# Performance work log

Hardware: AMD Instinct MI355X
Metric: run time of the kernel (lower is better)

## Reference

```python
import jax, jax.numpy as jnp
import numpy as np

N = 2048      # total nodes across all graphs
G = 16        # number of graphs
IN = 16       # input_dim
D = 256       # hidden_dim (d_model)
NH = 8        # num_heads
HD = D // NH  # head_dim
FF = 4 * D    # dim_feedforward
L = 4         # num_layers
LAT = 32      # latent_dim
BH = D // 2   # beta_head hidden
LN_EPS = 1e-5


def setup_inputs() -> dict:
    key = jax.random.key(0)
    ks = jax.random.split(key, 32)

    def w(k, shape, fan_in):
        return jax.random.normal(k, shape, jnp.float32) * (1.0 / np.sqrt(fan_in))

    inp = {
        "x": jax.random.normal(ks[0], (N, IN), jnp.float32),
        "coords": jax.random.normal(ks[1], (N, 3), jnp.float32),
        "batch": jnp.sort(jax.random.randint(ks[2], (N,), 0, G)).astype(jnp.int32),
        # input projection
        "Wi": w(ks[3], (IN, D), IN), "bi": jnp.zeros((D,), jnp.float32),
        # per-layer transformer params, stacked on leading layer dim
        "qkv_w": w(ks[4], (L, D, 3 * D), D), "qkv_b": jnp.zeros((L, 3 * D), jnp.float32),
        "out_w": w(ks[5], (L, D, D), D),     "out_b": jnp.zeros((L, D), jnp.float32),
        "ff1_w": w(ks[6], (L, D, FF), D),    "ff1_b": jnp.zeros((L, FF), jnp.float32),
        "ff2_w": w(ks[7], (L, FF, D), FF),   "ff2_b": jnp.zeros((L, D), jnp.float32),
        "ln1_s": jnp.ones((L, D), jnp.float32), "ln1_b": jnp.zeros((L, D), jnp.float32),
        "ln2_s": jnp.ones((L, D), jnp.float32), "ln2_b": jnp.zeros((L, D), jnp.float32),
        # heads
        "lat_w": w(ks[8], (D, LAT), D), "lat_b": jnp.zeros((LAT,), jnp.float32),
        "b1_w": w(ks[9], (D, BH), D),   "b1_b": jnp.zeros((BH,), jnp.float32),
        "b2_w": w(ks[10], (BH, 1), BH), "b2_b": jnp.zeros((1,), jnp.float32),
    }
    return inp


def _layer_norm(h, s, b):
    m = jnp.mean(h, axis=-1, keepdims=True)
    v = jnp.mean(jnp.square(h - m), axis=-1, keepdims=True)
    return (h - m) * jax.lax.rsqrt(v + LN_EPS) * s + b


def _forward(x, batch, Wi, bi, qkv_w, qkv_b, out_w, out_b, ff1_w, ff1_b,
             ff2_w, ff2_b, ln1_s, ln1_b, ln2_s, ln2_b, lat_w, lat_b,
             b1_w, b1_b, b2_w, b2_b):
    n = x.shape[0]
    h = x @ Wi + bi  # [N, D]
    # the per-graph python loop in torch == block-diagonal attention mask
    attn_bias = jnp.where(batch[:, None] == batch[None, :], 0.0, -1e9).astype(h.dtype)  # [N, N]
    scale = 1.0 / np.sqrt(HD)
    for l in range(L):
        qkv = h @ qkv_w[l] + qkv_b[l]                 # [N, 3D]
        q, k, v = jnp.split(qkv, 3, axis=-1)
        q = q.reshape(n, NH, HD)
        k = k.reshape(n, NH, HD)
        v = v.reshape(n, NH, HD)
        scores = jnp.einsum('nhd,mhd->hnm', q, k) * scale + attn_bias[None]  # [H, N, N]
        a = jax.nn.softmax(scores, axis=-1)
        o = jnp.einsum('hnm,mhd->nhd', a, v).reshape(n, D)
        o = o @ out_w[l] + out_b[l]
        h = _layer_norm(h + o, ln1_s[l], ln1_b[l])     # post-norm (torch default)
        f = jax.nn.relu(h @ ff1_w[l] + ff1_b[l]) @ ff2_w[l] + ff2_b[l]
        h = _layer_norm(h + f, ln2_s[l], ln2_b[l])
    lat = h @ lat_w + lat_b                            # [N, LAT]
    norm = jnp.maximum(jnp.linalg.norm(lat, axis=-1, keepdims=True), 1e-12)
    lat = lat / norm * np.sqrt(LAT)
    beta = jax.nn.sigmoid(jax.nn.relu(h @ b1_w + b1_b) @ b2_w + b2_b)  # [N, 1]
    beta = jnp.clip(beta, 1e-6, 1.0 - 1e-6)
    return beta, lat


def reference(x, coords, batch, Wi, bi, qkv_w, qkv_b, out_w, out_b,
              ff1_w, ff1_b, ff2_w, ff2_b, ln1_s, ln1_b, ln2_s, ln2_b,
              lat_w, lat_b, b1_w, b1_b, b2_w, b2_b):
    # coords is accepted (signature fidelity) but unused in the original forward
    del coords
    return _forward(x, batch, Wi, bi, qkv_w, qkv_b, out_w, out_b, ff1_w, ff1_b,
                    ff2_w, ff2_b, ln1_s, ln1_b, ln2_s, ln2_b, lat_w, lat_b,
                    b1_w, b1_b, b2_w, b2_b)
```

## Files before the change

### kernel.cpp

```cpp
#include <hip/hip_runtime.h>
#include <hip/hip_bf16.h>

typedef __attribute__((ext_vector_type(8))) short bf16x8;
typedef __attribute__((ext_vector_type(4))) float f32x4;

__device__ inline float wave_sum64(float v) {
#pragma unroll
  for (int m = 32; m >= 1; m >>= 1) v += __shfl_xor(v, m, 64);
  return v;
}
__device__ inline ushort f2bf(float f) {
  uint u = __float_as_uint(f);
  return (ushort)((u + 0x7FFFu + ((u >> 16) & 1u)) >> 16);
}

__global__ __launch_bounds__(256) void pack_inproj(
    const float* __restrict__ qkv_w, const float* __restrict__ out_w,
    const float* __restrict__ ff1_w, const float* __restrict__ ff2_w,
    const float* __restrict__ b1_w, const float* __restrict__ lat_w,
    short* __restrict__ qkv_t, short* __restrict__ out_t,
    short* __restrict__ ff1_t, short* __restrict__ ff2_t,
    short* __restrict__ b1_t, short* __restrict__ lat_t,
    const int* __restrict__ batch, int* __restrict__ starts, int* __restrict__ meta,
    const float* __restrict__ x, const float* __restrict__ Wi,
    const float* __restrict__ bi, float* __restrict__ h, short* __restrict__ hb) {
  int t = blockIdx.x;
  __shared__ float tile[32][33];

  if (t >= 3113) {
    const int row = t - 3113;
    const int j = threadIdx.x;
    float* xs = &tile[0][0];
    if (j < 16) xs[j] = x[(size_t)row * 16 + j];
    __syncthreads();
    float acc = bi[j];
#pragma unroll
    for (int k = 0; k < 16; ++k) acc += xs[k] * Wi[k * 256 + j];
    h[(size_t)row * 256 + j] = acc;
    hb[(size_t)row * 256 + j] = (short)f2bf(acc);
    return;
  }
  if (t == 3112) {
    for (int i = threadIdx.x; i < 2048; i += 256) {
      int b = batch[i];
      if (i == 0) {
        for (int g = 0; g <= b; ++g) starts[g] = 0;
      } else {
        int bp = batch[i - 1];
        for (int g = bp + 1; g <= b; ++g) starts[g] = i;
      }
      if (i == 2047) {
        for (int g = b + 1; g <= 16; ++g) starts[g] = 2048;
      }
    }
    __syncthreads();
    if (threadIdx.x == 0) {
      int nt = 0;
      for (int g = 0; g < 16; ++g) {
        const int js = starts[g], je = starts[g + 1];
        for (int q0 = js; q0 < je; q0 += 16) {
          meta[1 + nt * 3] = q0;
          meta[2 + nt * 3] = js;
          meta[3 + nt * 3] = je;
          ++nt;
        }
      }
      meta[0] = nt;
    }
    return;
  }
  const float* src;
  short* dst;
  int Kd, Nd, rem;
  if (t < 768) {
    int l = t / 192; rem = t % 192; Kd = 256; Nd = 768;
    src = qkv_w + (size_t)l * Kd * Nd; dst = qkv_t + (size_t)l * Nd * Kd;
  } else if (t < 1024) {
    t -= 768; int l = t / 64; rem = t % 64; Kd = 256; Nd = 256;
    src = out_w + (size_t)l * Kd * Nd; dst = out_t + (size_t)l * Nd * Kd;
  } else if (t < 2048) {
    t -= 1024; int l = t / 256; rem = t % 256; Kd = 256; Nd = 1024;
    src = ff1_w + (size_t)l * Kd * Nd; dst = ff1_t + (size_t)l * Nd * Kd;
  } else if (t < 3072) {
    t -= 2048; int l = t / 256; rem = t % 256; Kd = 1024; Nd = 256;
    src = ff2_w + (size_t)l * Kd * Nd; dst = ff2_t + (size_t)l * Nd * Kd;
  } else if (t < 3104) {
    rem = t - 3072; Kd = 256; Nd = 128; src = b1_w; dst = b1_t;
  } else {
    rem = t - 3104; Kd = 256; Nd = 32; src = lat_w; dst = lat_t;
  }
  const int ntn = Nd / 32;
  const int kt = rem / ntn, nt = rem % ntn;
  const int tx = threadIdx.x & 31, ty = threadIdx.x >> 5;
#pragma unroll
  for (int r = 0; r < 4; ++r) {
    int k = kt * 32 + ty + r * 8;
    tile[ty + r * 8][tx] = src[(size_t)k * Nd + nt * 32 + tx];
  }
  __syncthreads();
#pragma unroll
  for (int r = 0; r < 4; ++r) {
    int n = nt * 32 + ty + r * 8;
    dst[(size_t)n * Kd + kt * 32 + tx] = (short)f2bf(tile[tx][ty + r * 8]);
  }
}

template <int ACT, int P, int VT>
__global__ __launch_bounds__(256) void gemm_bf16(
    const short* __restrict__ A, const short* __restrict__ Bt,
    const float* __restrict__ bias, float* __restrict__ Cf, short* __restrict__ Cb,
    short* __restrict__ vtg, int M, int N, int K, int kpb) {
  __shared__ short As[64 * 128];
  __shared__ short Bs[64 * 128];

  const int t = threadIdx.x;
  const int bm = blockIdx.y, bn = blockIdx.x, bz = blockIdx.z;
  const int srow = t >> 2, sq = t & 3;
  const int lane = t & 63, wid = t >> 6;
  const int wr = wid >> 1, wc = wid & 1;
  const int fr = lane & 15, fs = lane >> 4;
  const int rx = srow & 7;

  f32x4 acc[2][2];
#pragma unroll
  for (int m = 0; m < 2; ++m)
#pragma unroll
    for (int n = 0; n < 2; ++n) acc[m][n] = (f32x4){0.f, 0.f, 0.f, 0.f};

  const int kbase = bz * kpb;
  const short* ap = A + (size_t)(bm * 64 + srow) * K + kbase;
  const int ng = bn * 64 + srow;
  const short* bp = Bt + (size_t)ng * K + kbase;
  const int ar0 = wr * 32 + fr, ar1 = ar0 + 16;
  const int bc0 = wc * 32 + fr, bc1 = bc0 + 16;

  for (int k0 = 0; k0 < kpb; k0 += 128) {
    bf16x8 av[4], bv[4];
#pragma unroll
    for (int i = 0; i < 4; ++i) av[i] = *(const bf16x8*)(ap + k0 + (sq * 4 + i) * 8);
    if (ng < N) {
#pragma unroll
      for (int i = 0; i < 4; ++i) bv[i] = *(const bf16x8*)(bp + k0 + (sq * 4 + i) * 8);
    } else {
#pragma unroll
      for (int i = 0; i < 4; ++i) bv[i] = (bf16x8){0, 0, 0, 0, 0, 0, 0, 0};
    }
    __syncthreads();
#pragma unroll
    for (int i = 0; i < 4; ++i) {
      const int s = sq * 4 + i;
      *(bf16x8*)(As + srow * 128 + ((s ^ rx) * 8)) = av[i];
      *(bf16x8*)(Bs + srow * 128 + ((s ^ rx) * 8)) = bv[i];
    }
    __syncthreads();
#pragma unroll
    for (int ks = 0; ks < 4; ++ks) {
      const int u = ks * 4 + fs;
      bf16x8 a0 = *(const bf16x8*)(As + ar0 * 128 + ((u ^ (ar0 & 7)) * 8));
      bf16x8 a1 = *(const bf16x8*)(As + ar1 * 128 + ((u ^ (ar1 & 7)) * 8));
      bf16x8 b0 = *(const bf16x8*)(Bs + bc0 * 128 + ((u ^ (bc0 & 7)) * 8));
      bf16x8 b1 = *(const bf16x8*)(Bs + bc1 * 128 + ((u ^ (bc1 & 7)) * 8));
      acc[0][0] = __builtin_amdgcn_mfma_f32_16x16x32_bf16(a0, b0, acc[0][0], 0, 0, 0);
      acc[0][1] = __builtin_amdgcn_mfma_f32_16x16x32_bf16(a0, b1, acc[0][1], 0, 0, 0);
      acc[1][0] = __builtin_amdgcn_mfma_f32_16x16x32_bf16(a1, b0, acc[1][0], 0, 0, 0);
      acc[1][1] = __builtin_amdgcn_mfma_f32_16x16x32_bf16(a1, b1, acc[1][1], 0, 0, 0);
    }
  }

  if (P == 0) {
    if (!(VT && bn >= 8)) {
#pragma unroll
      for (int n = 0; n < 2; ++n) {
        const int col = bn * 64 + wc * 32 + n * 16 + fr;
        if (col < N) {
          const float bvv = bias[col];
#pragma unroll
          for (int m = 0; m < 2; ++m) {
            const int rbase = bm * 64 + wr * 32 + m * 16 + fs * 4;
#pragma unroll
            for (int j = 0; j < 4; ++j) {
              float v = acc[m][n][j] + bvv;
              if (ACT == 1) v = fmaxf(v, 0.f);
              Cb[(size_t)(rbase + j) * N + col] = (short)f2bf(v);
            }
          }
        }
      }
    }
    if (VT && bn >= 8) {
      short* tr = As;
      __syncthreads();
#pragma unroll
      for (int n = 0; n < 2; ++n) {
        const int c = wc * 32 + n * 16 + fr;
        const float bvv = bias[bn * 64 + c];
#pragma unroll
        for (int m = 0; m < 2; ++m)
#pragma unroll
          for (int j = 0; j < 4; ++j) {
            const int r = wr * 32 + m * 16 + fs * 4 + j;
            tr[c * 68 + r] = (short)f2bf(acc[m][n][j] + bvv);
          }
      }
      __syncthreads();
      const int tx = t & 63, ty = t >> 6;
      const int d0 = bn * 64 - 512, rb = bm * 64;
#pragma unroll
      for (int r = 0; r < 16; ++r) {
        const int d = ty * 16 + r;
        vtg[(size_t)(d0 + d) * 2048 + rb + tx] = tr[d * 68 + tx];
      }
    }
  } else {
#pragma unroll
    for (int n = 0; n < 2; ++n) {
      const int col = bn * 64 + wc * 32 + n * 16 + fr;
      const float bvv = (bz == 0) ? bias[col] : 0.f;
#pragma unroll
      for (int m = 0; m < 2; ++m) {
        const int rbase = bm * 64 + wr * 32 + m * 16 + fs * 4;
#pragma unroll
        for (int j = 0; j < 4; ++j) {
          Cf[(size_t)(bz * M + rbase + j) * N + col] = acc[m][n][j] + bvv;
        }
      }
    }
  }
}

__global__ __launch_bounds__(512) void attn_fused(
    const short* __restrict__ qkv, const short* __restrict__ vtg,
    const int* __restrict__ meta, const short* __restrict__ out_t,
    const float* __restrict__ outb, const float* __restrict__ lns,
    const float* __restrict__ lnb, float* __restrict__ h, short* __restrict__ hb) {
  __shared__ short Ot[8][16][40];
  __shared__ float redS[8][16], redQ[8][16];
  const int w = threadIdx.x >> 6;
  const int tile = blockIdx.x;
  const bool active = (tile < meta[0]);
  const int lane = threadIdx.x & 63;
  const int fr = lane & 15, fs = lane >> 4;
  const int q0 = active ? meta[1 + tile * 3] : 0;
  const int js = active ? meta[2 + tile * 3] : 0;
  const int je = active ? meta[3 + tile * 3] : 0;
  const int jbase = js & ~15;
  const int njt = active ? ((je - jbase + 15) >> 4) : 0;
  const float scale = 0.17677669529663687f;

  const int qrow = min(q0 + fr, 2047);
  const bf16x8 qf = *(const bf16x8*)(qkv + (size_t)qrow * 768 + w * 32 + fs * 8);
  const int jeq = (q0 + fr < je) ? je : 0;

  f32x4 s[16];
#pragma unroll
  for (int jt = 0; jt < 16; ++jt)
    s[jt] = (f32x4){-3.0e38f, -3.0e38f, -3.0e38f, -3.0e38f};

#pragma unroll
  for (int jt = 0; jt < 16; ++jt) {
    if (jt < njt) {
      const int krow = min(jbase + jt * 16 + fr, 2047);
      const bf16x8 kf = *(const bf16x8*)(qkv + (size_t)krow * 768 + 256 + w * 32 + fs * 8);
      s[jt] = __builtin_amdgcn_mfma_f32_16x16x32_bf16(
          kf, qf, (f32x4){0.f, 0.f, 0.f, 0.f}, 0, 0, 0);
    }
  }
  float mx = -3.0e38f;
#pragma unroll
  for (int jt = 0; jt < 16; ++jt) {
    if (jt < njt) {
#pragma unroll
      for (int jj = 0; jj < 4; ++jj) {
        const int j = jbase + jt * 16 + fs * 4 + jj;
        const bool valid = (j >= js) && (j < jeq);
        s[jt][jj] = valid ? s[jt][jj] * scale : -3.0e38f;
        mx = fmaxf(mx, s[jt][jj]);
      }
    }
  }
  mx = fmaxf(mx, __shfl_xor(mx, 16, 64));
  mx = fmaxf(mx, __shfl_xor(mx, 32, 64));
  float l = 0.f;
#pragma unroll
  for (int jt = 0; jt < 16; ++jt) {
#pragma unroll
    for (int jj = 0; jj < 4; ++jj) {
      const float p = __expf(s[jt][jj] - mx);
      s[jt][jj] = p;
      l += p;
    }
  }
  l += __shfl_xor(l, 16, 64);
  l += __shfl_xor(l, 32, 64);

  f32x4 oa[2];
  oa[0] = (f32x4){0.f, 0.f, 0.f, 0.f};
  oa[1] = (f32x4){0.f, 0.f, 0.f, 0.f};
#pragma unroll
  for (int p2 = 0; p2 < 8; ++p2) {
    if (p2 * 2 < njt) {
      bf16x8 pa;
      pa[0] = (short)f2bf(s[p2 * 2][0]);     pa[1] = (short)f2bf(s[p2 * 2][1]);
      pa[2] = (short)f2bf(s[p2 * 2][2]);     pa[3] = (short)f2bf(s[p2 * 2][3]);
      pa[4] = (short)f2bf(s[p2 * 2 + 1][0]); pa[5] = (short)f2bf(s[p2 * 2 + 1][1]);
      pa[6] = (short)f2bf(s[p2 * 2 + 1][2]); pa[7] = (short)f2bf(s[p2 * 2 + 1][3]);
      const int jb0 = min(jbase + p2 * 32 + fs * 4, 2044);
      const int jb1 = min(jbase + p2 * 32 + 16 + fs * 4, 2044);
#pragma unroll
      for (int nt = 0; nt < 2; ++nt) {
        const short* vrow = vtg + (size_t)(w * 32 + nt * 16 + fr) * 2048;
        const short4 v0 = *(const short4*)(vrow + jb0);
        const short4 v1 = *(const short4*)(vrow + jb1);
        bf16x8 vf;
        vf[0] = v0.x; vf[1] = v0.y; vf[2] = v0.z; vf[3] = v0.w;
        vf[4] = v1.x; vf[5] = v1.y; vf[6] = v1.z; vf[7] = v1.w;
        oa[nt] = __builtin_amdgcn_mfma_f32_16x16x32_bf16(pa, vf, oa[nt], 0, 0, 0);
      }
    }
  }

#pragma unroll
  for (int jj = 0; jj < 4; ++jj) {
    const float lq = __shfl(l, fs * 4 + jj, 64);
    const float inv = (lq > 0.f) ? (1.f / lq) : 0.f;
    const int q = fs * 4 + jj;
    Ot[w][q][fr] = (short)f2bf(oa[0][jj] * inv);
    Ot[w][q][16 + fr] = (short)f2bf(oa[1][jj] * inv);
  }
  __syncthreads();

  f32x4 acc2[2];
  acc2[0] = (f32x4){0.f, 0.f, 0.f, 0.f};
  acc2[1] = (f32x4){0.f, 0.f, 0.f, 0.f};
#pragma unroll
  for (int ks = 0; ks < 8; ++ks) {
    const bf16x8 afrag = *(const bf16x8*)&Ot[ks][fr][fs * 8];
#pragma unroll
    for (int nt2 = 0; nt2 < 2; ++nt2) {
      const int col_row = (w * 2 + nt2) * 16 + fr;
      const bf16x8 bfrag =
          *(const bf16x8*)(out_t + (size_t)col_row * 256 + ks * 32 + fs * 8);
      acc2[nt2] = __builtin_amdgcn_mfma_f32_16x16x32_bf16(afrag, bfrag, acc2[nt2], 0, 0, 0);
    }
  }

  float d[2][4], ps[4], pq[4];
#pragma unroll
  for (int jj = 0; jj < 4; ++jj) {
    const int node = q0 + fs * 4 + jj;
    const int noder = min(node, 2047);
#pragma unroll
    for (int nt2 = 0; nt2 < 2; ++nt2) {
      const int col = w * 32 + nt2 * 16 + fr;
      d[nt2][jj] = acc2[nt2][jj] + outb[col] + h[(size_t)noder * 256 + col];
    }
    ps[jj] = d[0][jj] + d[1][jj];
    pq[jj] = d[0][jj] * d[0][jj] + d[1][jj] * d[1][jj];
#pragma unroll
    for (int m = 1; m <= 8; m <<= 1) {
      ps[jj] += __shfl_xor(ps[jj], m, 64);
      pq[jj] += __shfl_xor(pq[jj], m, 64);
    }
  }
  if (fr == 0) {
#pragma unroll
    for (int jj = 0; jj < 4; ++jj) {
      redS[w][fs * 4 + jj] = ps[jj];
      redQ[w][fs * 4 + jj] = pq[jj];
    }
  }
  __syncthreads();

#pragma unroll
  for (int jj = 0; jj < 4; ++jj) {
    const int row = fs * 4 + jj;
    float S = 0.f, Q = 0.f;
#pragma unroll
    for (int ww = 0; ww < 8; ++ww) { S += redS[ww][row]; Q += redQ[ww][row]; }
    const float mean = S * (1.f / 256.f);
    const float var = Q * (1.f / 256.f) - mean * mean;
    const float rs = rsqrtf(var + 1e-5f);
    const int node = q0 + row;
    if (active && node < je) {
#pragma unroll
      for (int nt2 = 0; nt2 < 2; ++nt2) {
        const int col = w * 32 + nt2 * 16 + fr;
        const float o = (d[nt2][jj] - mean) * rs * lns[col] + lnb[col];
        h[(size_t)node * 256 + col] = o;
        hb[(size_t)node * 256 + col] = (short)f2bf(o);
      }
    }
  }
}

template <int P>
__global__ __launch_bounds__(256) void ln_kernel(
    const float* __restrict__ base, const float* __restrict__ delta,
    const float* __restrict__ s, const float* __restrict__ b,
    float* __restrict__ outf, short* __restrict__ outb) {
  const int row = blockIdx.x * 4 + (threadIdx.x >> 6);
  const int lane = threadIdx.x & 63;
  float4 v = *(const float4*)(base + (size_t)row * 256 + lane * 4);
#pragma unroll
  for (int p = 0; p < P; ++p) {
    const float4 xb = *(const float4*)(delta + (size_t)(p * 2048 + row) * 256 + lane * 4);
    v.x += xb.x; v.y += xb.y; v.z += xb.z; v.w += xb.w;
  }
  float sum = wave_sum64(v.x + v.y + v.z + v.w);
  const float mean = sum * (1.f / 256.f);
  float4 d = make_float4(v.x - mean, v.y - mean, v.z - mean, v.w - mean);
  float sq = wave_sum64(d.x * d.x + d.y * d.y + d.z * d.z + d.w * d.w);
  const float rs = rsqrtf(sq * (1.f / 256.f) + 1e-5f);
  const float4 sv = *(const float4*)(s + lane * 4);
  const float4 bv = *(const float4*)(b + lane * 4);
  float4 o = make_float4(d.x * rs * sv.x + bv.x, d.y * rs * sv.y + bv.y,
                         d.z * rs * sv.z + bv.z, d.w * rs * sv.w + bv.w);
  *(float4*)(outf + (size_t)row * 256 + lane * 4) = o;
  short4 ob;
  ob.x = (short)f2bf(o.x); ob.y = (short)f2bf(o.y);
  ob.z = (short)f2bf(o.z); ob.w = (short)f2bf(o.w);
  *(short4*)(outb + (size_t)row * 256 + lane * 4) = ob;
}

__global__ __launch_bounds__(256) void heads_kernel(
    const short* __restrict__ A, const short* __restrict__ lat_t,
    const float* __restrict__ lat_b, float* __restrict__ lat_out,
    const short* __restrict__ b1_t, const float* __restrict__ b1b,
    const float* __restrict__ w2, const float* __restrict__ b2b,
    float* __restrict__ beta) {
  __shared__ short smem[64 * 128 * 2];
  const int t = threadIdx.x;
  const int lane = t & 63, w = t >> 6;
  const int fr = lane & 15, fs = lane >> 4;

  if (blockIdx.x < 32) {
    short* As = smem;
    short* Bs = smem + 64 * 128;
    const int bm = blockIdx.x;
    const int srow = t >> 2, sq = t & 3;
    const int rx = srow & 7;
    f32x4 acc[2];
    acc[0] = (f32x4){0.f, 0.f, 0.f, 0.f};
    acc[1] = (f32x4){0.f, 0.f, 0.f, 0.f};
    const short* ap = A + (size_t)(bm * 64 + srow) * 256;
    const short* bp = lat_t + (size_t)srow * 256;
    const int ar = w * 16 + fr;
    for (int k0 = 0; k0 < 256; k0 += 128) {
      bf16x8 av[4], bv[4];
#pragma unroll
      for (int i = 0; i < 4; ++i) av[i] = *(const bf16x8*)(ap + k0 + (sq * 4 + i) * 8);
      if (srow < 32) {
#pragma unroll
        for (int i = 0; i < 4; ++i) bv[i] = *(const bf16x8*)(bp + k0 + (sq * 4 + i) * 8);
      } else {
#pragma unroll
        for (int i = 0; i < 4; ++i) bv[i] = (bf16x8){0, 0, 0, 0, 0, 0, 0, 0};
      }
      __syncthreads();
#pragma unroll
      for (int i = 0; i < 4; ++i) {
        const int s = sq * 4 + i;
        *(bf16x8*)(As + srow * 128 + ((s ^ rx) * 8)) = av[i];
        *(bf16x8*)(Bs + srow * 128 + ((s ^ rx) * 8)) = bv[i];
      }
      __syncthreads();
#pragma unroll
      for (int ks = 0; ks < 4; ++ks) {
        const int u = ks * 4 + fs;
        bf16x8 a0 = *(const bf16x8*)(As + ar * 128 + ((u ^ (ar & 7)) * 8));
        bf16x8 b0 = *(const bf16x8*)(Bs + fr * 128 + ((u ^ (fr & 7)) * 8));
        bf16x8 b1 = *(const bf16x8*)(Bs + (16 + fr) * 128 + ((u ^ ((16 + fr) & 7)) * 8));
        acc[0] = __builtin_amdgcn_mfma_f32_16x16x32_bf16(a0, b0, acc[0], 0, 0, 0);
        acc[1] = __builtin_amdgcn_mfma_f32_16x16x32_bf16(a0, b1, acc[1], 0, 0, 0);
      }
    }
    const float b0v = lat_b[fr], b1v = lat_b[16 + fr];
#pragma unroll
    for (int j = 0; j < 4; ++j) {
      const int row = bm * 64 + w * 16 + fs * 4 + j;
      float v0 = acc[0][j] + b0v;
      float v1 = acc[1][j] + b1v;
      float ss = v0 * v0 + v1 * v1;
      ss += __shfl_xor(ss, 1, 64);
      ss += __shfl_xor(ss, 2, 64);
      ss += __shfl_xor(ss, 4, 64);
      ss += __shfl_xor(ss, 8, 64);
      const float inv = 5.656854249492381f / fmaxf(sqrtf(ss), 1e-12f);
      lat_out[(size_t)row * 32 + fr] = v0 * inv;
      lat_out[(size_t)row * 32 + 16 + fr] = v1 * inv;
    }
  } else {
    float* red = (float*)smem;
    const int rb = (blockIdx.x - 32) * 16;
    f32x4 acc[2];
    acc[0] = (f32x4){0.f, 0.f, 0.f, 0.f};
    acc[1] = (f32x4){0.f, 0.f, 0.f, 0.f};
    const short* ap = A + (size_t)(rb + fr) * 256;
    const short* bp = b1_t + (size_t)(w * 32 + fr) * 256;
    for (int k0 = 0; k0 < 256; k0 += 32) {
      const bf16x8 af = *(const bf16x8*)(ap + k0 + fs * 8);
#pragma unroll
      for (int n = 0; n < 2; ++n) {
        const bf16x8 bf = *(const bf16x8*)(bp + (size_t)n * 16 * 256 + k0 + fs * 8);
        acc[n] = __builtin_amdgcn_mfma_f32_16x16x32_bf16(af, bf, acc[n], 0, 0, 0);
      }
    }
    const int c0 = w * 32 + fr, c1 = c0 + 16;
    const float b0 = b1b[c0], b1 = b1b[c1];
    const float w0 = w2[c0], w1 = w2[c1];
    float part[4];
#pragma unroll
    for (int j = 0; j < 4; ++j) {
      const float d0 = fmaxf(acc[0][j] + b0, 0.f);
      const float d1 = fmaxf(acc[1][j] + b1, 0.f);
      part[j] = d0 * w0 + d1 * w1;
#pragma unroll
      for (int m = 1; m <= 8; m <<= 1) part[j] += __shfl_xor(part[j], m, 64);
    }
    if (fr == 0) {
#pragma unroll
      for (int j = 0; j < 4; ++j) red[w * 16 + fs * 4 + j] = part[j];
    }
    __syncthreads();
    if (t < 16) {
      const float S = red[t] + red[16 + t] + red[32 + t] + red[48 + t] + b2b[0];
      float sgm = 1.f / (1.f + __expf(-S));
      sgm = fminf(fmaxf(sgm, 1e-6f), 1.f - 1e-6f);
      beta[rb + t] = sgm;
    }
  }
}

extern "C" void kernel_launch(void* const* d_in, const int* in_sizes, int n_in,
                              void* d_out, int out_size, void* d_ws, size_t ws_size,
                              hipStream_t stream) {
  const int N = 2048, D = 256, FF = 1024, L = 4;

  const float* x     = (const float*)d_in[0];
  const int*   batch = (const int*)d_in[2];
  const float* Wi    = (const float*)d_in[3];
  const float* bi    = (const float*)d_in[4];
  const float* qkv_w = (const float*)d_in[5];
  const float* qkv_b = (const float*)d_in[6];
  const float* out_w = (const float*)d_in[7];
  const float* out_b = (const float*)d_in[8];
  const float* ff1_w = (const float*)d_in[9];
  const float* ff1_b = (const float*)d_in[10];
  const float* ff2_w = (const float*)d_in[11];
  const float* ff2_b = (const float*)d_in[12];
  const float* ln1_s = (const float*)d_in[13];
  const float* ln1_b = (const float*)d_in[14];
  const float* ln2_s = (const float*)d_in[15];
  const float* ln2_b = (const float*)d_in[16];
  const float* lat_w = (const float*)d_in[17];
  const float* lat_b = (const float*)d_in[18];
  const float* b1_w  = (const float*)d_in[19];
  const float* b1_b  = (const float*)d_in[20];
  const float* b2_w  = (const float*)d_in[21];
  const float* b2_b  = (const float*)d_in[22];

  float* ws = (float*)d_ws;
  float* h      = ws;
  float* tmp    = h + (size_t)N * D;
  int*  starts  = (int*)(tmp + (size_t)4 * N * D);
  int*  meta    = starts + 32;
  short* hb     = (short*)(meta + 448);
  short* qkvb   = hb + (size_t)N * D;
  short* ffb    = qkvb + (size_t)N * 3 * D;
  short* vtg    = ffb + (size_t)N * FF;
  short* qkv_t  = vtg + (size_t)256 * 2048;
  short* out_t  = qkv_t + (size_t)L * 768 * 256;
  short* ff1_t  = out_t + (size_t)L * 256 * 256;
  short* ff2_t  = ff1_t + (size_t)L * 1024 * 256;
  short* b1_t   = ff2_t + (size_t)L * 256 * 1024;
  short* lat_t  = b1_t + (size_t)128 * 256;

  float* beta_out = (float*)d_out;
  float* lat_out  = beta_out + N;

  pack_inproj<<<3113 + 2048, 256, 0, stream>>>(
      qkv_w, out_w, ff1_w, ff2_w, b1_w, lat_w,
      qkv_t, out_t, ff1_t, ff2_t, b1_t, lat_t,
      batch, starts, meta, x, Wi, bi, h, hb);

  for (int l = 0; l < L; ++l) {
    gemm_bf16<0, 0, 1><<<dim3(12, 32, 1), 256, 0, stream>>>(
        hb, qkv_t + (size_t)l * 768 * 256, qkv_b + (size_t)l * 768,
        nullptr, qkvb, vtg, N, 768, 256, 256);
    attn_fused<<<144, 512, 0, stream>>>(
        qkvb, vtg, meta, out_t + (size_t)l * 256 * 256, out_b + (size_t)l * 256,
        ln1_s + (size_t)l * D, ln1_b + (size_t)l * D, h, hb);
    gemm_bf16<1, 0, 0><<<dim3(16, 32, 1), 256, 0, stream>>>(
        hb, ff1_t + (size_t)l * FF * 256, ff1_b + (size_t)l * FF,
        nullptr, ffb, nullptr, N, FF, 256, 256);
    gemm_bf16<0, 4, 0><<<dim3(4, 32, 4), 256, 0, stream>>>(
        ffb, ff2_t + (size_t)l * 256 * FF, ff2_b + (size_t)l * 256,
        tmp, nullptr, nullptr, N, 256, 1024, 256);
    ln_kernel<4><<<N / 4, 256, 0, stream>>>(
        h, tmp, ln2_s + (size_t)l * D, ln2_b + (size_t)l * D, h, hb);
  }

  heads_kernel<<<160, 256, 0, stream>>>(hb, lat_t, lat_b, lat_out,
                                        b1_t, b1_b, b2_w, b2_b, beta_out);
}
```

Measured before the change: 190.5 us.

## Fuse FF1, ReLU, FF2, residual and LayerNorm into one per-row-tile kernel

Replaces the FF1 GEMM, the split-K FF2 GEMM and the LayerNorm kernel with a single kernel per 16-row tile. The ReLU intermediate is held in shared memory and the residual-plus-LayerNorm epilogue is done in registers. This removes two launches per layer and the global round trips of the 1024-wide intermediate and the split-K partials. In exchange, only 128 blocks run, weights are read straight from global memory without LDS tiling, and every block re-reads the full FF weights. The generic GEMM is also specialised into a QKV-only kernel.

```diff
diff --git a/kernel.cpp b/kernel.cpp
--- a/kernel.cpp
+++ b/kernel.cpp
@@ -105,16 +105,15 @@
   }
 }
 
-template <int ACT, int P, int VT>
-__global__ __launch_bounds__(256) void gemm_bf16(
+__global__ __launch_bounds__(256) void gemm_qkv(
     const short* __restrict__ A, const short* __restrict__ Bt,
-    const float* __restrict__ bias, float* __restrict__ Cf, short* __restrict__ Cb,
-    short* __restrict__ vtg, int M, int N, int K, int kpb) {
+    const float* __restrict__ bias, short* __restrict__ Cb,
+    short* __restrict__ vtg, int N, int K) {
   __shared__ short As[64 * 128];
   __shared__ short Bs[64 * 128];
 
   const int t = threadIdx.x;
-  const int bm = blockIdx.y, bn = blockIdx.x, bz = blockIdx.z;
+  const int bm = blockIdx.y, bn = blockIdx.x;
   const int srow = t >> 2, sq = t & 3;
   const int lane = t & 63, wid = t >> 6;
   const int wr = wid >> 1, wc = wid & 1;
@@ -127,24 +126,18 @@
 #pragma unroll
     for (int n = 0; n < 2; ++n) acc[m][n] = (f32x4){0.f, 0.f, 0.f, 0.f};
 
-  const int kbase = bz * kpb;
-  const short* ap = A + (size_t)(bm * 64 + srow) * K + kbase;
+  const short* ap = A + (size_t)(bm * 64 + srow) * K;
   const int ng = bn * 64 + srow;
-  const short* bp = Bt + (size_t)ng * K + kbase;
+  const short* bp = Bt + (size_t)ng * K;
   const int ar0 = wr * 32 + fr, ar1 = ar0 + 16;
   const int bc0 = wc * 32 + fr, bc1 = bc0 + 16;
 
-  for (int k0 = 0; k0 < kpb; k0 += 128) {
+  for (int k0 = 0; k0 < K; k0 += 128) {
     bf16x8 av[4], bv[4];
 #pragma unroll
     for (int i = 0; i < 4; ++i) av[i] = *(const bf16x8*)(ap + k0 + (sq * 4 + i) * 8);
-    if (ng < N) {
-#pragma unroll
-      for (int i = 0; i < 4; ++i) bv[i] = *(const bf16x8*)(bp + k0 + (sq * 4 + i) * 8);
-    } else {
-#pragma unroll
-      for (int i = 0; i < 4; ++i) bv[i] = (bf16x8){0, 0, 0, 0, 0, 0, 0, 0};
-    }
+#pragma unroll
+    for (int i = 0; i < 4; ++i) bv[i] = *(const bf16x8*)(bp + k0 + (sq * 4 + i) * 8);
     __syncthreads();
 #pragma unroll
     for (int i = 0; i < 4; ++i) {
@@ -167,63 +160,42 @@
     }
   }
 
-  if (P == 0) {
-    if (!(VT && bn >= 8)) {
-#pragma unroll
-      for (int n = 0; n < 2; ++n) {
-        const int col = bn * 64 + wc * 32 + n * 16 + fr;
-        if (col < N) {
-          const float bvv = bias[col];
-#pragma unroll
-          for (int m = 0; m < 2; ++m) {
-            const int rbase = bm * 64 + wr * 32 + m * 16 + fs * 4;
-#pragma unroll
-            for (int j = 0; j < 4; ++j) {
-              float v = acc[m][n][j] + bvv;
-              if (ACT == 1) v = fmaxf(v, 0.f);
-              Cb[(size_t)(rbase + j) * N + col] = (short)f2bf(v);
-            }
-          }
-        }
-      }
-    }
-    if (VT && bn >= 8) {
-      short* tr = As;
-      __syncthreads();
-#pragma unroll
-      for (int n = 0; n < 2; ++n) {
-        const int c = wc * 32 + n * 16 + fr;
-        const float bvv = bias[bn * 64 + c];
-#pragma unroll
-        for (int m = 0; m < 2; ++m)
-#pragma unroll
-          for (int j = 0; j < 4; ++j) {
-            const int r = wr * 32 + m * 16 + fs * 4 + j;
-            tr[c * 68 + r] = (short)f2bf(acc[m][n][j] + bvv);
-          }
-      }
-      __syncthreads();
-      const int tx = t & 63, ty = t >> 6;
-      const int d0 = bn * 64 - 512, rb = bm * 64;
-#pragma unroll
-      for (int r = 0; r < 16; ++r) {
-        const int d = ty * 16 + r;
-        vtg[(size_t)(d0 + d) * 2048 + rb + tx] = tr[d * 68 + tx];
-      }
-    }
-  } else {
+  if (bn < 8) {
 #pragma unroll
     for (int n = 0; n < 2; ++n) {
       const int col = bn * 64 + wc * 32 + n * 16 + fr;
-      const float bvv = (bz == 0) ? bias[col] : 0.f;
+      const float bvv = bias[col];
 #pragma unroll
       for (int m = 0; m < 2; ++m) {
         const int rbase = bm * 64 + wr * 32 + m * 16 + fs * 4;
 #pragma unroll
         for (int j = 0; j < 4; ++j) {
-          Cf[(size_t)(bz * M + rbase + j) * N + col] = acc[m][n][j] + bvv;
+          Cb[(size_t)(rbase + j) * N + col] = (short)f2bf(acc[m][n][j] + bvv);
         }
       }
+    }
+  } else {
+    short* tr = As;
+    __syncthreads();
+#pragma unroll
+    for (int n = 0; n < 2; ++n) {
+      const int c = wc * 32 + n * 16 + fr;
+      const float bvv = bias[bn * 64 + c];
+#pragma unroll
+      for (int m = 0; m < 2; ++m)
+#pragma unroll
+        for (int j = 0; j < 4; ++j) {
+          const int r = wr * 32 + m * 16 + fs * 4 + j;
+          tr[c * 68 + r] = (short)f2bf(acc[m][n][j] + bvv);
+        }
+    }
+    __syncthreads();
+    const int tx = t & 63, ty = t >> 6;
+    const int d0 = bn * 64 - 512, rb = bm * 64;
+#pragma unroll
+    for (int r = 0; r < 16; ++r) {
+      const int d = ty * 16 + r;
+      vtg[(size_t)(d0 + d) * 2048 + rb + tx] = tr[d * 68 + tx];
     }
   }
 }
@@ -393,33 +365,95 @@
   }
 }
 
-template <int P>
-__global__ __launch_bounds__(256) void ln_kernel(
-    const float* __restrict__ base, const float* __restrict__ delta,
-    const float* __restrict__ s, const float* __restrict__ b,
-    float* __restrict__ outf, short* __restrict__ outb) {
-  const int row = blockIdx.x * 4 + (threadIdx.x >> 6);
+__global__ __launch_bounds__(512) void ff_fused(
+    const short* __restrict__ hb_in, const short* __restrict__ ff1_t,
+    const float* __restrict__ ff1b, const short* __restrict__ ff2_t,
+    const float* __restrict__ ff2b, const float* __restrict__ lns,
+    const float* __restrict__ lnb, float* __restrict__ h, short* __restrict__ hb) {
+  __shared__ short Ff[16][1036];
+  __shared__ float redS[8][16], redQ[8][16];
+  const int w = threadIdx.x >> 6;
   const int lane = threadIdx.x & 63;
-  float4 v = *(const float4*)(base + (size_t)row * 256 + lane * 4);
-#pragma unroll
-  for (int p = 0; p < P; ++p) {
-    const float4 xb = *(const float4*)(delta + (size_t)(p * 2048 + row) * 256 + lane * 4);
-    v.x += xb.x; v.y += xb.y; v.z += xb.z; v.w += xb.w;
-  }
-  float sum = wave_sum64(v.x + v.y + v.z + v.w);
-  const float mean = sum * (1.f / 256.f);
-  float4 d = make_float4(v.x - mean, v.y - mean, v.z - mean, v.w - mean);
-  float sq = wave_sum64(d.x * d.x + d.y * d.y + d.z * d.z + d.w * d.w);
-  const float rs = rsqrtf(sq * (1.f / 256.f) + 1e-5f);
-  const float4 sv = *(const float4*)(s + lane * 4);
-  const float4 bv = *(const float4*)(b + lane * 4);
-  float4 o = make_float4(d.x * rs * sv.x + bv.x, d.y * rs * sv.y + bv.y,
-                         d.z * rs * sv.z + bv.z, d.w * rs * sv.w + bv.w);
-  *(float4*)(outf + (size_t)row * 256 + lane * 4) = o;
-  short4 ob;
-  ob.x = (short)f2bf(o.x); ob.y = (short)f2bf(o.y);
-  ob.z = (short)f2bf(o.z); ob.w = (short)f2bf(o.w);
-  *(short4*)(outb + (size_t)row * 256 + lane * 4) = ob;
+  const int fr = lane & 15, fs = lane >> 4;
+  const int rb = blockIdx.x * 16;
+
+  const short* ap = hb_in + (size_t)(rb + fr) * 256 + fs * 8;
+#pragma unroll
+  for (int nt = 0; nt < 8; ++nt) {
+    const int colr = w * 128 + nt * 16 + fr;
+    f32x4 acc = (f32x4){0.f, 0.f, 0.f, 0.f};
+    const short* bp = ff1_t + (size_t)colr * 256 + fs * 8;
+#pragma unroll
+    for (int k0 = 0; k0 < 256; k0 += 32) {
+      const bf16x8 af = *(const bf16x8*)(ap + k0);
+      const bf16x8 bf = *(const bf16x8*)(bp + k0);
+      acc = __builtin_amdgcn_mfma_f32_16x16x32_bf16(af, bf, acc, 0, 0, 0);
+    }
+    const float bv = ff1b[colr];
+#pragma unroll
+    for (int j = 0; j < 4; ++j) {
+      Ff[fs * 4 + j][colr] = (short)f2bf(fmaxf(acc[j] + bv, 0.f));
+    }
+  }
+  __syncthreads();
+
+  f32x4 acc2[2];
+  acc2[0] = (f32x4){0.f, 0.f, 0.f, 0.f};
+  acc2[1] = (f32x4){0.f, 0.f, 0.f, 0.f};
+  for (int k0 = 0; k0 < 1024; k0 += 32) {
+    const bf16x8 af = *(const bf16x8*)&Ff[fr][k0 + fs * 8];
+#pragma unroll
+    for (int nt2 = 0; nt2 < 2; ++nt2) {
+      const int colr = w * 32 + nt2 * 16 + fr;
+      const bf16x8 bf = *(const bf16x8*)(ff2_t + (size_t)colr * 1024 + k0 + fs * 8);
+      acc2[nt2] = __builtin_amdgcn_mfma_f32_16x16x32_bf16(af, bf, acc2[nt2], 0, 0, 0);
+    }
+  }
+
+  float d[2][4], ps[4], pq[4];
+#pragma unroll
+  for (int jj = 0; jj < 4; ++jj) {
+    const int row = rb + fs * 4 + jj;
+#pragma unroll
+    for (int nt2 = 0; nt2 < 2; ++nt2) {
+      const int col = w * 32 + nt2 * 16 + fr;
+      d[nt2][jj] = acc2[nt2][jj] + ff2b[col] + h[(size_t)row * 256 + col];
+    }
+    ps[jj] = d[0][jj] + d[1][jj];
+    pq[jj] = d[0][jj] * d[0][jj] + d[1][jj] * d[1][jj];
+#pragma unroll
+    for (int m = 1; m <= 8; m <<= 1) {
+      ps[jj] += __shfl_xor(ps[jj], m, 64);
+      pq[jj] += __shfl_xor(pq[jj], m, 64);
+    }
+  }
+  if (fr == 0) {
+#pragma unroll
+    for (int jj = 0; jj < 4; ++jj) {
+      redS[w][fs * 4 + jj] = ps[jj];
+      redQ[w][fs * 4 + jj] = pq[jj];
+    }
+  }
+  __syncthreads();
+
+#pragma unroll
+  for (int jj = 0; jj < 4; ++jj) {
+    const int row = fs * 4 + jj;
+    float S = 0.f, Q = 0.f;
+#pragma unroll
+    for (int ww = 0; ww < 8; ++ww) { S += redS[ww][row]; Q += redQ[ww][row]; }
+    const float mean = S * (1.f / 256.f);
+    const float var = Q * (1.f / 256.f) - mean * mean;
+    const float rs = rsqrtf(var + 1e-5f);
+    const int node = rb + row;
+#pragma unroll
+    for (int nt2 = 0; nt2 < 2; ++nt2) {
+      const int col = w * 32 + nt2 * 16 + fr;
+      const float o = (d[nt2][jj] - mean) * rs * lns[col] + lnb[col];
+      h[(size_t)node * 256 + col] = o;
+      hb[(size_t)node * 256 + col] = (short)f2bf(o);
+    }
+  }
 }
 
 __global__ __launch_bounds__(256) void heads_kernel(
@@ -561,13 +595,11 @@
 
   float* ws = (float*)d_ws;
   float* h      = ws;
-  float* tmp    = h + (size_t)N * D;
-  int*  starts  = (int*)(tmp + (size_t)4 * N * D);
+  int*  starts  = (int*)(h + (size_t)N * D);
   int*  meta    = starts + 32;
   short* hb     = (short*)(meta + 448);
   short* qkvb   = hb + (size_t)N * D;
-  short* ffb    = qkvb + (size_t)N * 3 * D;
-  short* vtg    = ffb + (size_t)N * FF;
+  short* vtg    = qkvb + (size_t)N * 3 * D;
   short* qkv_t  = vtg + (size_t)256 * 2048;
   short* out_t  = qkv_t + (size_t)L * 768 * 256;
   short* ff1_t  = out_t + (size_t)L * 256 * 256;
@@ -584,20 +616,16 @@
       batch, starts, meta, x, Wi, bi, h, hb);
 
   for (int l = 0; l < L; ++l) {
-    gemm_bf16<0, 0, 1><<<dim3(12, 32, 1), 256, 0, stream>>>(
+    gemm_qkv<<<dim3(12, 32), 256, 0, stream>>>(
         hb, qkv_t + (size_t)l * 768 * 256, qkv_b + (size_t)l * 768,
-        nullptr, qkvb, vtg, N, 768, 256, 256);
+        qkvb, vtg, 768, 256);
     attn_fused<<<144, 512, 0, stream>>>(
         qkvb, vtg, meta, out_t + (size_t)l * 256 * 256, out_b + (size_t)l * 256,
         ln1_s + (size_t)l * D, ln1_b + (size_t)l * D, h, hb);
-    gemm_bf16<1, 0, 0><<<dim3(16, 32, 1), 256, 0, stream>>>(
+    ff_fused<<<128, 512, 0, stream>>>(
         hb, ff1_t + (size_t)l * FF * 256, ff1_b + (size_t)l * FF,
-        nullptr, ffb, nullptr, N, FF, 256, 256);
-    gemm_bf16<0, 4, 0><<<dim3(4, 32, 4), 256, 0, stream>>>(
-        ffb, ff2_t + (size_t)l * 256 * FF, ff2_b + (size_t)l * 256,
-        tmp, nullptr, nullptr, N, 256, 1024, 256);
-    ln_kernel<4><<<N / 4, 256, 0, stream>>>(
-        h, tmp, ln2_s + (size_t)l * D, ln2_b + (size_t)l * D, h, hb);
+        ff2_t + (size_t)l * 256 * FF, ff2_b + (size_t)l * 256,
+        ln2_s + (size_t)l * D, ln2_b + (size_t)l * D, h, hb);
   }
 
   heads_kernel<<<160, 256, 0, stream>>>(hb, lat_t, lat_b, lat_out,
```

After: 284.8 us. 49.5% more time.
